# Kernel optimization log

Hardware: AMD Instinct MI355X
Metric: run time of the kernel (lower is better)

## Reference

```python
import jax, jax.numpy as jnp
import numpy as np

DIM = 512
HEADS = 8
DIM_HEAD = 64
INNER = HEADS * DIM_HEAD  # 512
LN_EPS = 1e-5


def setup_inputs() -> dict:
    key = jax.random.key(0)
    ks = jax.random.split(key, 6)
    b, n = 2, 2048
    x = jax.random.normal(ks[0], (b, n, DIM), dtype=jnp.float32)
    # to_qkv: Linear(dim, inner*3, bias=False); torch weight is [out,in], apply as x @ W.T
    w_qkv = jax.random.normal(ks[1], (3 * INNER, DIM), dtype=jnp.float32) * (DIM ** -0.5)
    reattn_w = jax.random.normal(ks[2], (HEADS, HEADS), dtype=jnp.float32)
    ln_g = jnp.ones((HEADS,), dtype=jnp.float32)
    ln_b = jnp.zeros((HEADS,), dtype=jnp.float32)
    w_out = jax.random.normal(ks[3], (DIM, INNER), dtype=jnp.float32) * (INNER ** -0.5)
    b_out = jnp.zeros((DIM,), dtype=jnp.float32)
    return {"x": x, "w_qkv": w_qkv, "reattn_w": reattn_w,
            "ln_g": ln_g, "ln_b": ln_b, "w_out": w_out, "b_out": b_out}


def reference(x, w_qkv, reattn_w, ln_g, ln_b, w_out, b_out):
    b, n, _ = x.shape
    scale = DIM_HEAD ** -0.5
    qkv = x @ w_qkv.T  # [b, n, 3*inner]
    q, k, v = jnp.split(qkv, 3, axis=-1)
    # b n (h d) -> b h n d
    split_heads = lambda t: t.reshape(b, n, HEADS, DIM_HEAD).transpose(0, 2, 1, 3)
    q, k, v = split_heads(q), split_heads(k), split_heads(v)
    dots = jnp.einsum('bhid,bhjd->bhij', q, k) * scale
    attn = jax.nn.softmax(dots, axis=-1)
    # re-attention: cross-head mixing then LayerNorm over head dim
    attn = jnp.einsum('bhij,hg->bgij', attn, reattn_w)
    a = attn.transpose(0, 2, 3, 1)  # b i j h
    mu = jnp.mean(a, axis=-1, keepdims=True)
    var = jnp.mean((a - mu) ** 2, axis=-1, keepdims=True)
    a = (a - mu) * jax.lax.rsqrt(var + LN_EPS) * ln_g + ln_b
    attn = a.transpose(0, 3, 1, 2)  # b h i j
    out = jnp.einsum('bhij,bhjd->bhid', attn, v)
    out = out.transpose(0, 2, 1, 3).reshape(b, n, INNER)
    out = out @ w_out.T + b_out  # dropout p=0 -> identity
    return out
```

## Files before the change

### kernel.cpp

```cpp
#include <hip/hip_runtime.h>
#include <hip/hip_bf16.h>


typedef __attribute__((ext_vector_type(8))) short bfx8;
typedef __attribute__((ext_vector_type(4))) float f32x4;
typedef unsigned short u16;
typedef unsigned int u32;

#define QSCALE 0.18033688011112042f

static __device__ inline u16 f2bf(float f) {
  union { float f; unsigned u; } cv; cv.f = f;
  unsigned u = cv.u;
  u += 0x7fffu + ((u >> 16) & 1u);
  return (u16)(u >> 16);
}
static __device__ inline u32 cvtpk(float lo, float hi) {
  u32 d; asm("v_cvt_pk_bf16_f32 %0, %1, %2" : "=v"(d) : "v"(lo), "v"(hi)); return d;
}
static __device__ inline float fexp2(float x) {
  float r; asm("v_exp_f32 %0, %1" : "=v"(r) : "v"(x)); return r;
}
static __device__ inline float flog2(float x) {
  float r; asm("v_log_f32 %0, %1" : "=v"(r) : "v"(x)); return r;
}
static __device__ inline uint4 pk8(const float* p) {
  float4 a = *(const float4*)p, b = *(const float4*)(p + 4);
  return make_uint4(cvtpk(a.x, a.y), cvtpk(a.z, a.w), cvtpk(b.x, b.y), cvtpk(b.z, b.w));
}

__global__ __launch_bounds__(256) void gemm_qkv(
    const float* __restrict__ A, const float* __restrict__ B,
    u16* __restrict__ qb, u16* __restrict__ kb, u16* __restrict__ vtb,
    float4* __restrict__ zeroF) {
  __shared__ u16 As[64 * 32];
  __shared__ u16 Bs[128 * 32];
  const int bid = blockIdx.x, t = threadIdx.x;
  for (int e = bid * 256 + t; e < 524288; e += 196608)
    zeroF[e] = make_float4(0.f, 0.f, 0.f, 0.f);
  const int swzb = (bid & 7) * 96 + (bid >> 3);
  const int m0 = (swzb / 12) * 64, n0 = (swzb % 12) * 128;
  const int lane = t & 63, w = t >> 6;
  const int li = lane & 15, lg = lane >> 4;
  const int rowA = t >> 2, kb8 = (t & 3) * 8;
  f32x4 acc[4][2] = {};
  for (int k0 = 0; k0 < 512; k0 += 32) {
    __syncthreads();
    *(uint4*)&As[rowA * 32 + kb8]        = pk8(&A[(size_t)(m0 + rowA) * 512 + k0 + kb8]);
    *(uint4*)&Bs[rowA * 32 + kb8]        = pk8(&B[(size_t)(n0 + rowA) * 512 + k0 + kb8]);
    *(uint4*)&Bs[(rowA + 64) * 32 + kb8] = pk8(&B[(size_t)(n0 + rowA + 64) * 512 + k0 + kb8]);
    __syncthreads();
    bfx8 af[4], bf_[2];
#pragma unroll
    for (int mi = 0; mi < 4; mi++)
      af[mi] = *(const bfx8*)&As[(mi * 16 + li) * 32 + lg * 8];
#pragma unroll
    for (int ni = 0; ni < 2; ni++)
      bf_[ni] = *(const bfx8*)&Bs[(w * 32 + ni * 16 + li) * 32 + lg * 8];
#pragma unroll
    for (int mi = 0; mi < 4; mi++)
#pragma unroll
      for (int ni = 0; ni < 2; ni++)
        acc[mi][ni] = __builtin_amdgcn_mfma_f32_16x16x32_bf16(af[mi], bf_[ni], acc[mi][ni], 0, 0, 0);
  }
#pragma unroll
  for (int mi = 0; mi < 4; mi++) {
#pragma unroll
    for (int ni = 0; ni < 2; ni++) {
      const int nc  = n0 + w * 32 + ni * 16 + li;
      const int mrb = m0 + mi * 16 + lg * 4;
      const int part = nc >> 9, within = nc & 511;
      const int h = within >> 6, d = within & 63;
      const int bb = mrb >> 11, ii = mrb & 2047;
      if (part == 0) {
#pragma unroll
        for (int r = 0; r < 4; r++)
          qb[(((size_t)bb * 8 + h) * 2048 + ii + r) * 64 + d] = f2bf(acc[mi][ni][r] * QSCALE);
      } else if (part == 1) {
#pragma unroll
        for (int r = 0; r < 4; r++)
          kb[(((size_t)bb * 8 + h) * 2048 + ii + r) * 64 + d] = f2bf(acc[mi][ni][r]);
      } else {
        ushort4 u;
        u.x = f2bf(acc[mi][ni][0]); u.y = f2bf(acc[mi][ni][1]);
        u.z = f2bf(acc[mi][ni][2]); u.w = f2bf(acc[mi][ni][3]);
        *(ushort4*)&vtb[(((size_t)bb * 8 + h) * 64 + d) * 2048 + ii] = u;
      }
    }
  }
}

__global__ __launch_bounds__(256) void passA(
    const u16* __restrict__ qb, const u16* __restrict__ kb,
    float2* __restrict__ statp) {
  const int bid = blockIdx.x;
  const int swzb = (bid & 7) * 512 + (bid >> 3);
  const int bx = swzb & 31, bh = (swzb >> 5) & 15, js = swzb >> 9;
  const int t = threadIdx.x, lane = t & 63, w = t >> 6;
  const int i0 = bx * 64 + w * 16;
  const int li = lane & 15, lg = lane >> 4;
  const u16* Qh = qb + ((size_t)bh * 2048 + i0 + li) * 64;
  const u16* Kb = kb + (size_t)bh * 2048 * 64;
  const bfx8 q0 = *(const bfx8*)&Qh[lg * 8];
  const bfx8 q1 = *(const bfx8*)&Qh[32 + lg * 8];
  float m = -1e30f, l = 0.f;
  const int jbeg = js * 256, jend = jbeg + 256;
  for (int j0 = jbeg; j0 < jend; j0 += 32) {
    const u16* KhA = Kb + (size_t)(j0 + li) * 64;
    const u16* KhB = KhA + 16 * 64;
    bfx8 a0 = *(const bfx8*)&KhA[lg * 8];
    bfx8 a1 = *(const bfx8*)&KhA[32 + lg * 8];
    bfx8 b0 = *(const bfx8*)&KhB[lg * 8];
    bfx8 b1 = *(const bfx8*)&KhB[32 + lg * 8];
    __builtin_amdgcn_sched_barrier(0);
    f32x4 sa = {0.f, 0.f, 0.f, 0.f}, sb = {0.f, 0.f, 0.f, 0.f};
    sa = __builtin_amdgcn_mfma_f32_16x16x32_bf16(a0, q0, sa, 0, 0, 0);
    sa = __builtin_amdgcn_mfma_f32_16x16x32_bf16(a1, q1, sa, 0, 0, 0);
    sb = __builtin_amdgcn_mfma_f32_16x16x32_bf16(b0, q0, sb, 0, 0, 0);
    sb = __builtin_amdgcn_mfma_f32_16x16x32_bf16(b1, q1, sb, 0, 0, 0);
    float mt = fmaxf(fmaxf(fmaxf(sa[0], sa[1]), fmaxf(sa[2], sa[3])),
                     fmaxf(fmaxf(sb[0], sb[1]), fmaxf(sb[2], sb[3])));
    float mn = fmaxf(m, mt);
    float es = (fexp2(sa[0] - mn) + fexp2(sa[1] - mn)) + (fexp2(sa[2] - mn) + fexp2(sa[3] - mn))
             + (fexp2(sb[0] - mn) + fexp2(sb[1] - mn)) + (fexp2(sb[2] - mn) + fexp2(sb[3] - mn));
    l = fmaf(l, fexp2(m - mn), es);
    m = mn;
  }
  for (int off = 16; off < 64; off <<= 1) {
    float mo = __shfl_xor(m, off, 64);
    float lo = __shfl_xor(l, off, 64);
    float mn = fmaxf(m, mo);
    l = l * fexp2(m - mn) + lo * fexp2(mo - mn);
    m = mn;
  }
  if (lane < 16) statp[(size_t)js * 32768 + (size_t)bh * 2048 + i0 + li] = make_float2(m, l);
}

__global__ __launch_bounds__(512) void kFused(
    const u16* __restrict__ qb, const u16* __restrict__ kb,
    const u16* __restrict__ vtb, const float2* __restrict__ statp,
    const float* __restrict__ Wmix, const float* __restrict__ lng,
    const float* __restrict__ lnb, float* __restrict__ innerF) {
  __shared__ __align__(16) u16 Spk[64 * 512];
  __shared__ __align__(16) u16 A2h[8 * 64 * 72];
  __shared__ float stMs[64 * 8];
  const int t = threadIdx.x, lane = t & 63, w = t >> 6;
  const int li = lane & 15, lg = lane >> 4;
  const int ig = blockIdx.x * 64, b = blockIdx.y, j0 = blockIdx.z * 512;

  float wm_[8][8], lng_[8], lnb_[8];
#pragma unroll
  for (int h = 0; h < 8; h++)
#pragma unroll
    for (int g = 0; g < 8; g++) wm_[h][g] = Wmix[h * 8 + g];
#pragma unroll
  for (int g = 0; g < 8; g++) { lng_[g] = lng[g]; lnb_[g] = lnb[g]; }

  {
    const int i = t >> 3, h = t & 7;
    const size_t idx = ((size_t)(b * 8 + h)) * 2048 + ig + i;
    float m = -1e30f, l = 0.f;
#pragma unroll
    for (int z = 0; z < 8; z++) {
      const float2 a = statp[(size_t)z * 32768 + idx];
      const float mn = fmaxf(m, a.x);
      l = l * fexp2(m - mn) + a.y * fexp2(a.x - mn);
      m = mn;
    }
    stMs[i * 8 + h] = m + flog2(l);
  }

  bfx8 qf[4][2];
#pragma unroll
  for (int ii = 0; ii < 4; ii++)
#pragma unroll
    for (int ks = 0; ks < 2; ks++)
      qf[ii][ks] = *(const bfx8*)&qb[(((size_t)(b * 8 + w)) * 2048 + ig + ii * 16 + li) * 64
                                     + ks * 32 + lg * 8];
  __syncthreads();
  float stMp[4];
#pragma unroll
  for (int ii = 0; ii < 4; ii++) stMp[ii] = stMs[(ii * 16 + li) * 8 + w];

  f32x4 pacc[4][4] = {};
  const int mixI = t >> 3, mixJ8 = (t & 7) * 8;
  const int mixSwz = (mixI & 7) << 3;

  bfx8 kf[4][2];
#pragma unroll
  for (int ji = 0; ji < 4; ji++)
#pragma unroll
    for (int ks = 0; ks < 2; ks++)
      kf[ji][ks] = *(const bfx8*)&kb[(((size_t)(b * 8 + w)) * 2048 + j0 + ji * 16 + li) * 64
                                     + ks * 32 + lg * 8];

  for (int jt = j0; jt < j0 + 512; jt += 64) {
#pragma unroll
    for (int ii = 0; ii < 4; ii++) {
      f32x4 s[4] = {};
#pragma unroll
      for (int ji = 0; ji < 4; ji++) {
        s[ji] = __builtin_amdgcn_mfma_f32_16x16x32_bf16(kf[ji][0], qf[ii][0], s[ji], 0, 0, 0);
        s[ji] = __builtin_amdgcn_mfma_f32_16x16x32_bf16(kf[ji][1], qf[ii][1], s[ji], 0, 0, 0);
      }
      const int i = ii * 16 + li;
      const int swzI = (i & 7) << 3;
#pragma unroll
      for (int ji = 0; ji < 4; ji++) {
        const float p0 = fexp2(s[ji][0] - stMp[ii]);
        const float p1 = fexp2(s[ji][1] - stMp[ii]);
        const float p2 = fexp2(s[ji][2] - stMp[ii]);
        const float p3 = fexp2(s[ji][3] - stMp[ii]);
        const int x = (ji * 16 + lg * 4) ^ swzI;
        *(uint2*)&Spk[i * 512 + w * 64 + x] = make_uint2(cvtpk(p0, p1), cvtpk(p2, p3));
      }
    }
    __syncthreads();
    bfx8 vf0[4], vf1[4];
#pragma unroll
    for (int dt = 0; dt < 4; dt++) {
      vf0[dt] = *(const bfx8*)&vtb[(((size_t)(b * 8 + w)) * 64 + dt * 16 + li) * 2048
                                   + jt + lg * 8];
      vf1[dt] = *(const bfx8*)&vtb[(((size_t)(b * 8 + w)) * 64 + dt * 16 + li) * 2048
                                   + jt + 32 + lg * 8];
    }
    {
      const int jn = (jt + 64 < j0 + 512) ? jt + 64 : j0;
#pragma unroll
      for (int ji = 0; ji < 4; ji++)
#pragma unroll
        for (int ks = 0; ks < 2; ks++)
          kf[ji][ks] = *(const bfx8*)&kb[(((size_t)(b * 8 + w)) * 2048 + jn + ji * 16 + li) * 64
                                         + ks * 32 + lg * 8];
    }
    __builtin_amdgcn_sched_barrier(0);
    {
      uint4 sv[8];
#pragma unroll
      for (int h = 0; h < 8; h++)
        sv[h] = *(const uint4*)&Spk[mixI * 512 + h * 64 + (mixJ8 ^ mixSwz)];
      u32 ogw[8][4];
      float tmp[8];
#pragma unroll
      for (int hf = 0; hf < 2; hf++) {
        float p[8][4];
#pragma unroll
        for (int h = 0; h < 8; h++) {
          const u32 va = hf ? sv[h].z : sv[h].x;
          const u32 vb = hf ? sv[h].w : sv[h].y;
          union { u32 u; float f; } c0, c1, c2, c3;
          c0.u = va << 16; c1.u = va & 0xffff0000u;
          c2.u = vb << 16; c3.u = vb & 0xffff0000u;
          p[h][0] = c0.f; p[h][1] = c1.f; p[h][2] = c2.f; p[h][3] = c3.f;
        }
#pragma unroll
        for (int e = 0; e < 4; e++) {
          float a_[8]; float sum = 0.f, sumsq = 0.f;
#pragma unroll
          for (int g = 0; g < 8; g++) {
            float acc = 0.f;
#pragma unroll
            for (int h = 0; h < 8; h++) acc = fmaf(p[h][e], wm_[h][g], acc);
            a_[g] = acc; sum += acc; sumsq = fmaf(acc, acc, sumsq);
          }
          const float mu = sum * 0.125f;
          const float var = fmaf(sumsq, 0.125f, -mu * mu);
          const float rs = rsqrtf(var + 1e-5f);
#pragma unroll
          for (int g = 0; g < 8; g++) {
            const float av = fmaf((a_[g] - mu) * rs, lng_[g], lnb_[g]);
            if (e & 1) ogw[g][hf * 2 + (e >> 1)] = cvtpk(tmp[g], av);
            else       tmp[g] = av;
          }
        }
      }
#pragma unroll
      for (int g = 0; g < 8; g++)
        *(uint4*)&A2h[g * 4608 + mixI * 72 + (mixJ8 ^ mixSwz)] =
            make_uint4(ogw[g][0], ogw[g][1], ogw[g][2], ogw[g][3]);
    }
    __syncthreads();
    __builtin_amdgcn_s_setprio(1);
#pragma unroll
    for (int iSub = 0; iSub < 4; iSub++) {
      const bfx8 af0 = *(const bfx8*)&A2h[w * 4608 + (iSub * 16 + li) * 72
                                          + ((lg * 8) ^ ((li & 7) << 3))];
#pragma unroll
      for (int dt = 0; dt < 4; dt++)
        pacc[iSub][dt] = __builtin_amdgcn_mfma_f32_16x16x32_bf16(af0, vf0[dt], pacc[iSub][dt], 0, 0, 0);
    }
#pragma unroll
    for (int iSub = 0; iSub < 4; iSub++) {
      const bfx8 af1 = *(const bfx8*)&A2h[w * 4608 + (iSub * 16 + li) * 72
                                          + ((32 + lg * 8) ^ ((li & 7) << 3))];
#pragma unroll
      for (int dt = 0; dt < 4; dt++)
        pacc[iSub][dt] = __builtin_amdgcn_mfma_f32_16x16x32_bf16(af1, vf1[dt], pacc[iSub][dt], 0, 0, 0);
    }
    __builtin_amdgcn_s_setprio(0);
  }
#pragma unroll
  for (int iSub = 0; iSub < 4; iSub++)
#pragma unroll
    for (int dt = 0; dt < 4; dt++)
#pragma unroll
      for (int r = 0; r < 4; r++)
        atomicAdd(&innerF[((size_t)b * 2048 + ig + iSub * 16 + lg * 4 + r) * 512
                          + w * 64 + dt * 16 + li],
                  pacc[iSub][dt][r]);
}

__global__ __launch_bounds__(256) void gemm_out(
    const float* __restrict__ A, const float* __restrict__ B,
    float* __restrict__ outf, const float* __restrict__ bias) {
  __shared__ u16 As[64 * 32];
  __shared__ u16 Bs[128 * 32];
  const int bid = blockIdx.x;
  const int swzb = (bid & 7) * 32 + (bid >> 3);
  const int m0 = (swzb >> 2) * 64, n0 = (swzb & 3) * 128;
  const int t = threadIdx.x, lane = t & 63, w = t >> 6;
  const int li = lane & 15, lg = lane >> 4;
  const int rowA = t >> 2, kb8 = (t & 3) * 8;
  f32x4 acc[4][2] = {};
  for (int k0 = 0; k0 < 512; k0 += 32) {
    __syncthreads();
    *(uint4*)&As[rowA * 32 + kb8]        = pk8(&A[(size_t)(m0 + rowA) * 512 + k0 + kb8]);
    *(uint4*)&Bs[rowA * 32 + kb8]        = pk8(&B[(size_t)(n0 + rowA) * 512 + k0 + kb8]);
    *(uint4*)&Bs[(rowA + 64) * 32 + kb8] = pk8(&B[(size_t)(n0 + rowA + 64) * 512 + k0 + kb8]);
    __syncthreads();
    bfx8 af[4], bf_[2];
#pragma unroll
    for (int mi = 0; mi < 4; mi++)
      af[mi] = *(const bfx8*)&As[(mi * 16 + li) * 32 + lg * 8];
#pragma unroll
    for (int ni = 0; ni < 2; ni++)
      bf_[ni] = *(const bfx8*)&Bs[(w * 32 + ni * 16 + li) * 32 + lg * 8];
#pragma unroll
    for (int mi = 0; mi < 4; mi++)
#pragma unroll
      for (int ni = 0; ni < 2; ni++)
        acc[mi][ni] = __builtin_amdgcn_mfma_f32_16x16x32_bf16(af[mi], bf_[ni], acc[mi][ni], 0, 0, 0);
  }
#pragma unroll
  for (int mi = 0; mi < 4; mi++) {
#pragma unroll
    for (int ni = 0; ni < 2; ni++) {
      const int nc  = n0 + w * 32 + ni * 16 + li;
      const int mrb = m0 + mi * 16 + lg * 4;
      const float bv = bias[nc];
#pragma unroll
      for (int r = 0; r < 4; r++)
        outf[(size_t)(mrb + r) * 512 + nc] = acc[mi][ni][r] + bv;
    }
  }
}

extern "C" void kernel_launch(void* const* d_in, const int* in_sizes, int n_in,
                              void* d_out, int out_size, void* d_ws, size_t ws_size,
                              hipStream_t stream) {
  const float* x      = (const float*)d_in[0];
  const float* w_qkv  = (const float*)d_in[1];
  const float* reattn = (const float*)d_in[2];
  const float* ln_g   = (const float*)d_in[3];
  const float* ln_b   = (const float*)d_in[4];
  const float* w_out  = (const float*)d_in[5];
  const float* b_out  = (const float*)d_in[6];
  float* out = (float*)d_out;
  char* ws = (char*)d_ws;
  float*  innerF= (float*)(ws + 0);
  u16*    qbf   = (u16*)(ws + 8388608);
  u16*    kbf   = (u16*)(ws + 12582912);
  u16*    vtb   = (u16*)(ws + 16777216);
  float2* statp = (float2*)(ws + 20971520);

  gemm_qkv<<<768, 256, 0, stream>>>(x, w_qkv, qbf, kbf, vtb, (float4*)innerF);
  passA<<<4096, 256, 0, stream>>>(qbf, kbf, statp);
  kFused<<<dim3(32, 2, 4), 512, 0, stream>>>(qbf, kbf, vtb, statp, reattn, ln_g, ln_b, innerF);
  gemm_out<<<256, 256, 0, stream>>>(innerF, w_out, out, b_out);
}
```

Baseline: 185.6 us.

## Halve kFused query tile to 32 rows with 4 waves each handling two heads

kFused now processes 32 query rows per block with 256 threads. Each of the 4 waves covers two heads instead of one, and the grid doubles to 512 blocks. The per-block LDS footprint drops, and the Spk row stride is padded to 520 to reduce bank conflicts. K fragments are no longer prefetched across iterations; K and V are loaded per head right before use, which may expose more memory latency while aiming for higher occupancy and better CU coverage.

```diff
diff --git a/kernel.cpp b/kernel.cpp
--- a/kernel.cpp
+++ b/kernel.cpp
@@ -8,6 +8,7 @@
 typedef unsigned int u32;
 
 #define QSCALE 0.18033688011112042f
+#define SPK_STRIDE 520
 
 static __device__ inline u16 f2bf(float f) {
   union { float f; unsigned u; } cv; cv.f = f;
@@ -136,17 +137,17 @@
   if (lane < 16) statp[(size_t)js * 32768 + (size_t)bh * 2048 + i0 + li] = make_float2(m, l);
 }
 
-__global__ __launch_bounds__(512) void kFused(
+__global__ __launch_bounds__(256) void kFused(
     const u16* __restrict__ qb, const u16* __restrict__ kb,
     const u16* __restrict__ vtb, const float2* __restrict__ statp,
     const float* __restrict__ Wmix, const float* __restrict__ lng,
     const float* __restrict__ lnb, float* __restrict__ innerF) {
-  __shared__ __align__(16) u16 Spk[64 * 512];
-  __shared__ __align__(16) u16 A2h[8 * 64 * 72];
-  __shared__ float stMs[64 * 8];
+  __shared__ __align__(16) u16 Spk[32 * SPK_STRIDE];
+  __shared__ __align__(16) u16 A2h[8 * 32 * 72];
+  __shared__ float stMs[32 * 8];
   const int t = threadIdx.x, lane = t & 63, w = t >> 6;
   const int li = lane & 15, lg = lane >> 4;
-  const int ig = blockIdx.x * 64, b = blockIdx.y, j0 = blockIdx.z * 512;
+  const int ig = blockIdx.x * 32, b = blockIdx.y, j0 = blockIdx.z * 512;
 
   float wm_[8][8], lng_[8], lnb_[8];
 #pragma unroll
@@ -170,75 +171,66 @@
     stMs[i * 8 + h] = m + flog2(l);
   }
 
-  bfx8 qf[4][2];
-#pragma unroll
-  for (int ii = 0; ii < 4; ii++)
-#pragma unroll
-    for (int ks = 0; ks < 2; ks++)
-      qf[ii][ks] = *(const bfx8*)&qb[(((size_t)(b * 8 + w)) * 2048 + ig + ii * 16 + li) * 64
-                                     + ks * 32 + lg * 8];
+  bfx8 qf[2][2][2];
+#pragma unroll
+  for (int hh = 0; hh < 2; hh++)
+#pragma unroll
+    for (int ii = 0; ii < 2; ii++)
+#pragma unroll
+      for (int ks = 0; ks < 2; ks++)
+        qf[hh][ii][ks] = *(const bfx8*)&qb[(((size_t)(b * 8 + w + hh * 4)) * 2048
+                                            + ig + ii * 16 + li) * 64 + ks * 32 + lg * 8];
   __syncthreads();
-  float stMp[4];
-#pragma unroll
-  for (int ii = 0; ii < 4; ii++) stMp[ii] = stMs[(ii * 16 + li) * 8 + w];
-
-  f32x4 pacc[4][4] = {};
+  float stMp[2][2];
+#pragma unroll
+  for (int hh = 0; hh < 2; hh++)
+#pragma unroll
+    for (int ii = 0; ii < 2; ii++)
+      stMp[hh][ii] = stMs[(ii * 16 + li) * 8 + w + hh * 4];
+
+  f32x4 pacc[2][2][4] = {};
   const int mixI = t >> 3, mixJ8 = (t & 7) * 8;
   const int mixSwz = (mixI & 7) << 3;
 
-  bfx8 kf[4][2];
-#pragma unroll
-  for (int ji = 0; ji < 4; ji++)
-#pragma unroll
-    for (int ks = 0; ks < 2; ks++)
-      kf[ji][ks] = *(const bfx8*)&kb[(((size_t)(b * 8 + w)) * 2048 + j0 + ji * 16 + li) * 64
-                                     + ks * 32 + lg * 8];
-
   for (int jt = j0; jt < j0 + 512; jt += 64) {
 #pragma unroll
-    for (int ii = 0; ii < 4; ii++) {
-      f32x4 s[4] = {};
-#pragma unroll
-      for (int ji = 0; ji < 4; ji++) {
-        s[ji] = __builtin_amdgcn_mfma_f32_16x16x32_bf16(kf[ji][0], qf[ii][0], s[ji], 0, 0, 0);
-        s[ji] = __builtin_amdgcn_mfma_f32_16x16x32_bf16(kf[ji][1], qf[ii][1], s[ji], 0, 0, 0);
+    for (int hh = 0; hh < 2; hh++) {
+      const int h = w + hh * 4;
+      bfx8 kf[4][2];
+#pragma unroll
+      for (int ji = 0; ji < 4; ji++)
+#pragma unroll
+        for (int ks = 0; ks < 2; ks++)
+          kf[ji][ks] = *(const bfx8*)&kb[(((size_t)(b * 8 + h)) * 2048 + jt + ji * 16 + li) * 64
+                                         + ks * 32 + lg * 8];
+      __builtin_amdgcn_sched_barrier(0);
+#pragma unroll
+      for (int ii = 0; ii < 2; ii++) {
+        f32x4 s[4] = {};
+#pragma unroll
+        for (int ji = 0; ji < 4; ji++) {
+          s[ji] = __builtin_amdgcn_mfma_f32_16x16x32_bf16(kf[ji][0], qf[hh][ii][0], s[ji], 0, 0, 0);
+          s[ji] = __builtin_amdgcn_mfma_f32_16x16x32_bf16(kf[ji][1], qf[hh][ii][1], s[ji], 0, 0, 0);
+        }
+        const int i = ii * 16 + li;
+        const int swzI = (i & 7) << 3;
+#pragma unroll
+        for (int ji = 0; ji < 4; ji++) {
+          const float p0 = fexp2(s[ji][0] - stMp[hh][ii]);
+          const float p1 = fexp2(s[ji][1] - stMp[hh][ii]);
+          const float p2 = fexp2(s[ji][2] - stMp[hh][ii]);
+          const float p3 = fexp2(s[ji][3] - stMp[hh][ii]);
+          const int x = (ji * 16 + lg * 4) ^ swzI;
+          *(uint2*)&Spk[i * SPK_STRIDE + h * 64 + x] = make_uint2(cvtpk(p0, p1), cvtpk(p2, p3));
+        }
       }
-      const int i = ii * 16 + li;
-      const int swzI = (i & 7) << 3;
-#pragma unroll
-      for (int ji = 0; ji < 4; ji++) {
-        const float p0 = fexp2(s[ji][0] - stMp[ii]);
-        const float p1 = fexp2(s[ji][1] - stMp[ii]);
-        const float p2 = fexp2(s[ji][2] - stMp[ii]);
-        const float p3 = fexp2(s[ji][3] - stMp[ii]);
-        const int x = (ji * 16 + lg * 4) ^ swzI;
-        *(uint2*)&Spk[i * 512 + w * 64 + x] = make_uint2(cvtpk(p0, p1), cvtpk(p2, p3));
-      }
-    }
-    __syncthreads();
-    bfx8 vf0[4], vf1[4];
-#pragma unroll
-    for (int dt = 0; dt < 4; dt++) {
-      vf0[dt] = *(const bfx8*)&vtb[(((size_t)(b * 8 + w)) * 64 + dt * 16 + li) * 2048
-                                   + jt + lg * 8];
-      vf1[dt] = *(const bfx8*)&vtb[(((size_t)(b * 8 + w)) * 64 + dt * 16 + li) * 2048
-                                   + jt + 32 + lg * 8];
-    }
-    {
-      const int jn = (jt + 64 < j0 + 512) ? jt + 64 : j0;
-#pragma unroll
-      for (int ji = 0; ji < 4; ji++)
-#pragma unroll
-        for (int ks = 0; ks < 2; ks++)
-          kf[ji][ks] = *(const bfx8*)&kb[(((size_t)(b * 8 + w)) * 2048 + jn + ji * 16 + li) * 64
-                                         + ks * 32 + lg * 8];
-    }
-    __builtin_amdgcn_sched_barrier(0);
+    }
+    __syncthreads();
     {
       uint4 sv[8];
 #pragma unroll
       for (int h = 0; h < 8; h++)
-        sv[h] = *(const uint4*)&Spk[mixI * 512 + h * 64 + (mixJ8 ^ mixSwz)];
+        sv[h] = *(const uint4*)&Spk[mixI * SPK_STRIDE + h * 64 + (mixJ8 ^ mixSwz)];
       u32 ogw[8][4];
       float tmp[8];
 #pragma unroll
@@ -276,38 +268,48 @@
       }
 #pragma unroll
       for (int g = 0; g < 8; g++)
-        *(uint4*)&A2h[g * 4608 + mixI * 72 + (mixJ8 ^ mixSwz)] =
+        *(uint4*)&A2h[g * 2304 + mixI * 72 + (mixJ8 ^ mixSwz)] =
             make_uint4(ogw[g][0], ogw[g][1], ogw[g][2], ogw[g][3]);
     }
     __syncthreads();
     __builtin_amdgcn_s_setprio(1);
 #pragma unroll
-    for (int iSub = 0; iSub < 4; iSub++) {
-      const bfx8 af0 = *(const bfx8*)&A2h[w * 4608 + (iSub * 16 + li) * 72
-                                          + ((lg * 8) ^ ((li & 7) << 3))];
+    for (int hh = 0; hh < 2; hh++) {
+      const int h = w + hh * 4;
+      bfx8 vf[2][4];
+#pragma unroll
+      for (int ks = 0; ks < 2; ks++)
+#pragma unroll
+        for (int dt = 0; dt < 4; dt++)
+          vf[ks][dt] = *(const bfx8*)&vtb[(((size_t)(b * 8 + h)) * 64 + dt * 16 + li) * 2048
+                                          + jt + ks * 32 + lg * 8];
+      __builtin_amdgcn_sched_barrier(0);
+#pragma unroll
+      for (int iSub = 0; iSub < 2; iSub++) {
+#pragma unroll
+        for (int ks = 0; ks < 2; ks++) {
+          const bfx8 af = *(const bfx8*)&A2h[h * 2304 + (iSub * 16 + li) * 72
+                                             + ((ks * 32 + lg * 8) ^ ((li & 7) << 3))];
+#pragma unroll
+          for (int dt = 0; dt < 4; dt++)
+            pacc[hh][iSub][dt] =
+                __builtin_amdgcn_mfma_f32_16x16x32_bf16(af, vf[ks][dt], pacc[hh][iSub][dt], 0, 0, 0);
+        }
+      }
+    }
+    __builtin_amdgcn_s_setprio(0);
+  }
+#pragma unroll
+  for (int hh = 0; hh < 2; hh++)
+#pragma unroll
+    for (int iSub = 0; iSub < 2; iSub++)
 #pragma unroll
       for (int dt = 0; dt < 4; dt++)
-        pacc[iSub][dt] = __builtin_amdgcn_mfma_f32_16x16x32_bf16(af0, vf0[dt], pacc[iSub][dt], 0, 0, 0);
-    }
-#pragma unroll
-    for (int iSub = 0; iSub < 4; iSub++) {
-      const bfx8 af1 = *(const bfx8*)&A2h[w * 4608 + (iSub * 16 + li) * 72
-                                          + ((32 + lg * 8) ^ ((li & 7) << 3))];
-#pragma unroll
-      for (int dt = 0; dt < 4; dt++)
-        pacc[iSub][dt] = __builtin_amdgcn_mfma_f32_16x16x32_bf16(af1, vf1[dt], pacc[iSub][dt], 0, 0, 0);
-    }
-    __builtin_amdgcn_s_setprio(0);
-  }
-#pragma unroll
-  for (int iSub = 0; iSub < 4; iSub++)
-#pragma unroll
-    for (int dt = 0; dt < 4; dt++)
-#pragma unroll
-      for (int r = 0; r < 4; r++)
-        atomicAdd(&innerF[((size_t)b * 2048 + ig + iSub * 16 + lg * 4 + r) * 512
-                          + w * 64 + dt * 16 + li],
-                  pacc[iSub][dt][r]);
+#pragma unroll
+        for (int r = 0; r < 4; r++)
+          atomicAdd(&innerF[((size_t)b * 2048 + ig + iSub * 16 + lg * 4 + r) * 512
+                            + (w + hh * 4) * 64 + dt * 16 + li],
+                    pacc[hh][iSub][dt][r]);
 }
 
 __global__ __launch_bounds__(256) void gemm_out(
@@ -375,6 +377,6 @@
 
   gemm_qkv<<<768, 256, 0, stream>>>(x, w_qkv, qbf, kbf, vtb, (float4*)innerF);
   passA<<<4096, 256, 0, stream>>>(qbf, kbf, statp);
-  kFused<<<dim3(32, 2, 4), 512, 0, stream>>>(qbf, kbf, vtb, statp, reattn, ln_g, ln_b, innerF);
+  kFused<<<dim3(64, 2, 4), 256, 0, stream>>>(qbf, kbf, vtb, statp, reattn, ln_g, ln_b, innerF);
   gemm_out<<<256, 256, 0, stream>>>(innerF, w_out, out, b_out);
 }
```

Result: slower. 189.8 us (+2.3%).
